# Kernel optimization log

Hardware: AMD Instinct MI355X
Metric: run time of the kernel (lower is better)

## Reference

```python
import jax, jax.numpy as jnp
import numpy as np

N, G = 10000, 200          # nodes, graphs
EL, EG = 160000, 500000    # local / global edges
S, V = 256, 64             # scalar / vector hidden dims
NA, NB = 16, 5             # atom types, bond types


def _lin(k, i, o):
    return (jax.random.normal(k, (i, o), jnp.float32) / np.sqrt(i))


def scatter_mean(vals, idx, num_segments):
    # vals: [N, ...]; idx: [N] int
    sums = jax.ops.segment_sum(vals, idx, num_segments=num_segments)
    cnt = jax.ops.segment_sum(jnp.ones((vals.shape[0],), vals.dtype), idx,
                              num_segments=num_segments)
    cnt = jnp.maximum(cnt, 1.0).reshape((-1,) + (1,) * (vals.ndim - 1))
    return sums / cnt


def calc_edge_attrs(edge_index, pos):
    src, tgt = edge_index[0], edge_index[1]
    r = pos[tgt] - pos[src]                      # [E,3]
    a = (pos[tgt] * pos[src]).sum(-1)            # [E]
    d = jnp.sqrt(jnp.clip((r ** 2).sum(-1), 1e-6))
    r_norm = r / d[:, None]
    return d, a, r_norm


def setup_inputs() -> dict:
    key = jax.random.key(0)
    ks = jax.random.split(key, 24)
    inp = {}
    inp["x"] = jax.random.normal(ks[0], (N, NA), jnp.float32)
    inp["t"] = jax.random.uniform(ks[1], (G, 1), jnp.float32)
    inp["pos"] = jax.random.normal(ks[2], (N, 3), jnp.float32)
    eil = jax.random.randint(ks[3], (2, EL), 0, N)
    eig = jax.random.randint(ks[4], (2, EG), 0, N)
    # avoid self-edges so edge distances are strictly positive (safe sqrt grads)
    eig = eig.at[1].set(jnp.where(eig[1] == eig[0], (eig[1] + 1) % N, eig[1]))
    eil = eil.at[1].set(jnp.where(eil[1] == eil[0], (eil[1] + 1) % N, eil[1]))
    inp["edge_index_local"] = eil
    inp["edge_index_global"] = eig
    inp["edge_attr_global"] = jax.random.normal(ks[5], (EG, NB), jnp.float32)
    inp["batch"] = jnp.sort(jax.random.randint(ks[6], (N,), 0, G))
    # learned parameters
    inp["W_time"], inp["b_time"] = _lin(ks[7], 1, S), jnp.zeros((S,), jnp.float32)
    inp["W_atom"], inp["b_atom"] = _lin(ks[8], NA, S), jnp.zeros((S,), jnp.float32)
    inp["W_at"], inp["b_at"] = _lin(ks[9], S, S), jnp.zeros((S,), jnp.float32)
    inp["W_shared"], inp["b_shared"] = _lin(ks[10], S, S), jnp.zeros((S,), jnp.float32)
    inp["W_b0"], inp["b_b0"] = _lin(ks[11], S + 1, S), jnp.zeros((S,), jnp.float32)
    inp["W_b1"], inp["b_b1"] = _lin(ks[12], S, 2 * NB), jnp.zeros((2 * NB,), jnp.float32)
    inp["W_coord"] = _lin(ks[13], V, 2)           # no bias
    inp["W_atoms"], inp["b_atoms"] = _lin(ks[14], S, 2 * NA), jnp.zeros((2 * NA,), jnp.float32)
    return inp


def reference(x, t, pos, edge_attr_global, W_time, b_time, W_atom, b_atom,
              W_at, b_at, W_shared, b_shared, W_b0, b_b0, W_b1, b_b1,
              W_coord, W_atoms, b_atoms,
              edge_index_local, edge_index_global, batch):
    # --- trunk: center positions, embed atoms + time ---
    pos = pos - scatter_mean(pos, batch, G)[batch]
    temb = t @ W_time + b_time                    # [G,S]
    tnode = temb[batch]                           # [N,S]
    s = x @ W_atom + b_atom
    s = (s + tnode) @ W_at + b_at                 # [N,S]
    # --- edge attrs (gather-compute pattern feeding the GNN) ---
    d_l, a_l, rn_l = calc_edge_attrs(edge_index_local, pos)
    d_g, a_g, rn_g = calc_edge_attrs(edge_index_global, pos)
    # GNN stand-in (identity on s, v, p): v initialized to zeros as in original
    v = jnp.zeros((N, 3, V), s.dtype)
    # --- prediction head ---
    s = jax.nn.silu(s @ W_shared + b_shared)
    j, i = edge_index_global[0], edge_index_global[1]
    d = jnp.sqrt(((pos[i] - pos[j]) ** 2).sum(-1, keepdims=True))  # [EG,1]
    edge = jnp.concatenate([s[i] + s[j], d], axis=-1)              # [EG,S+1]
    bonds = jax.nn.silu(edge @ W_b0 + b_b0) @ W_b1 + b_b1          # [EG,2*NB]
    bonds_pred, bonds_eps = bonds[:, :NB], bonds[:, NB:]
    coords = jnp.einsum('nkv,vo->nko', v, W_coord)                 # [N,3,2]
    coords = coords - scatter_mean(coords, batch, G)[batch]
    coords_eps0, coords_eps1 = coords[..., 0], coords[..., 1]      # [N,3]
    atoms = s @ W_atoms + b_atoms                                  # [N,2*NA]
    atoms_eps, atoms_pred = atoms[:, :NA], atoms[:, NA:]
    pos_c = pos - scatter_mean(pos, batch, G)[batch]
    coords_pred = pos_c + coords_eps1
    return (coords_pred, coords_eps0, atoms_pred, atoms_eps,
            bonds_pred, bonds_eps, d_l, rn_l, a_g, rn_g)
```

## Files before the change

kernel.cpp:

```cpp
#include <hip/hip_runtime.h>
#include <hip/hip_bf16.h>

typedef __hip_bfloat16 bf16;
typedef short bf16x8 __attribute__((ext_vector_type(8)));
typedef float f32x4 __attribute__((ext_vector_type(4)));
typedef float f32x2 __attribute__((ext_vector_type(2)));

#define N_NODES  10000
#define G_GRAPHS 200
#define EL_EDGES 160000
#define EG_EDGES 500000
#define S_DIM    256
#define APAD     264

#define BONDS_BLOCKS 15625
#define LOCAL_BLOCKS 625

#define WS_FLAG   0
#define WS_POSC   1024
#define WS_WD     31232
#define WS_BB0    31488
#define WS_BB1    34304
#define WS_WATOM  34560
#define WS_WTIME  38656
#define WS_BTIME  38912
#define WS_BATOM  39168
#define WS_BAT    39424
#define WS_BSH    39680
#define WS_BATOMS 39936
#define WS_T      40000
#define WS_X      40448
#define WT_AT     200448
#define WT_SH     233216
#define WT_B0     265984
#define WT_ATOMS  298752
#define WT_B1     302848
#define WS_H      304896
#define WS_END_FLOATS (WS_H + (N_NODES * S_DIM) / 4)

#define CHAN(S)    ((((S) >> 6) << 6) + (((S) & 3) << 4) + (((S) & 63) >> 2))
#define CHANINV(k) ((((k) >> 6) << 6) + (((k) & 15) << 2) + (((k) >> 4) & 3))

#define O_CPRED 0
#define O_CEPS  30000
#define O_APRED 60000
#define O_AEPS  220000
#define O_BPRED 380000
#define O_BEPS  2880000
#define O_DL    5380000
#define O_RNL   5540000
#define O_AG    6020000
#define O_RNG   6520000

__device__ __forceinline__ float b2f(bf16 v) { return __bfloat162float(v); }
__device__ __forceinline__ bf16  f2b(float v) { return __float2bfloat16(v); }
__device__ __forceinline__ unsigned short bbits(float v) {
    bf16 b = f2b(v);
    return *reinterpret_cast<unsigned short*>(&b);
}
__device__ __forceinline__ float ldin(const void* p, int idx, int isf32) {
    return isf32 ? ((const float*)p)[idx] : b2f(((const bf16*)p)[idx]);
}
__device__ __forceinline__ void stout(void* out, int f32o, size_t idx, float v) {
    if (f32o) ((float*)out)[idx] = v;
    else      ((bf16*)out)[idx]  = f2b(v);
}
__device__ __forceinline__ float silu(float p) {
    return p * __builtin_amdgcn_rcpf(1.0f + __expf(-p));
}
__device__ __forceinline__ int dtype_f32(const void* tt) {
    const unsigned short* q = (const unsigned short*)tt;
    int c = 0;
#pragma unroll
    for (int z = 0; z < 32; ++z) c += (q[z] >= 0x4000) ? 1 : 0;
    return c > 0;
}

__global__ void k_prep(const void* __restrict__ x, const void* __restrict__ tt,
                       const void* __restrict__ W_time, const void* __restrict__ b_time,
                       const void* __restrict__ W_atom, const void* __restrict__ b_atom,
                       const void* __restrict__ W_at, const void* __restrict__ b_at,
                       const void* __restrict__ W_shared, const void* __restrict__ b_shared,
                       const void* __restrict__ W_b0, const void* __restrict__ b_b0,
                       const void* __restrict__ W_b1, const void* __restrict__ b_b1,
                       const void* __restrict__ W_atoms, const void* __restrict__ b_atoms,
                       float* __restrict__ ws) {
    const int t = blockIdx.x * blockDim.x + threadIdx.x;
    const int f = dtype_f32(tt);
    if (t == 0) ws[WS_FLAG] = f ? 1.0f : 0.0f;
    if (t < 65536) {
        const int k = t >> 8, n = t & 255;
        ((unsigned short*)(ws + WT_AT))[n * 256 + k] = bbits(ldin(W_at, t, f));
        ((unsigned short*)(ws + WT_SH))[n * 256 + k] = bbits(ldin(W_shared, t, f));
        ((unsigned short*)(ws + WT_B0))[n * 256 + k] = bbits(ldin(W_b0, t, f));
    }
    if (t < 160000) ws[WS_X + t] = ldin(x, t, f);
    if (t < 8192) {
        const int k = t >> 5, n = t & 31;
        ((unsigned short*)(ws + WT_ATOMS))[n * 256 + k] = bbits(ldin(W_atoms, t, f));
    }
    if (t < 4096) ws[WS_WATOM + t] = ldin(W_atom, t, f);
    if (t < 2560) {
        const int k = t / 10, n = t - k * 10;
        ((unsigned short*)(ws + WT_B1))[n * 256 + CHANINV(k)] = bbits(ldin(W_b1, t, f));
    } else if (t < 4096) {
        ((unsigned short*)(ws + WT_B1))[t] = 0;
    }
    if (t < 256) {
        ws[WS_WD + t]    = ldin(W_b0, 65536 + CHAN(t), f);
        ws[WS_BB0 + t]   = ldin(b_b0, CHAN(t), f);
        ws[WS_WTIME + t] = ldin(W_time, t, f);
        ws[WS_BTIME + t] = ldin(b_time, t, f);
        ws[WS_BATOM + t] = ldin(b_atom, t, f);
        ws[WS_BAT + t]   = ldin(b_at, t, f);
        ws[WS_BSH + t]   = ldin(b_shared, t, f);
    }
    if (t < 200) ws[WS_T + t] = ldin(tt, t, f);
    if (t < 32)  ws[WS_BATOMS + t] = ldin(b_atoms, t, f);
    if (t < 16)  ws[WS_BB1 + t] = (t < 10) ? ldin(b_b1, t, f) : 0.0f;
}

__global__ void k_pos(const void* __restrict__ pos, const int* __restrict__ batch,
                      float* __restrict__ ws, void* __restrict__ out) {
    const int g = blockIdx.x;
    const int f32o = ws[WS_FLAG] != 0.0f;
    __shared__ int s_lo, s_hi;
    __shared__ float wsum[4][3];
    __shared__ float mean[3];
    if (threadIdx.x == 0) {
        int lo = 0, hi = N_NODES;
        while (lo < hi) { int m = (lo + hi) >> 1; if (batch[m] < g) lo = m + 1; else hi = m; }
        s_lo = lo;
        int lo2 = lo; hi = N_NODES;
        while (lo2 < hi) { int m = (lo2 + hi) >> 1; if (batch[m] < g + 1) lo2 = m + 1; else hi = m; }
        s_hi = lo2;
    }
    __syncthreads();
    const int lo = s_lo, hi = s_hi, cnt = hi - lo;
    float sx = 0.f, sy = 0.f, sz = 0.f;
    for (int n = lo + threadIdx.x; n < hi; n += 256) {
        sx += ldin(pos, n * 3 + 0, f32o);
        sy += ldin(pos, n * 3 + 1, f32o);
        sz += ldin(pos, n * 3 + 2, f32o);
    }
#pragma unroll
    for (int off = 32; off > 0; off >>= 1) {
        sx += __shfl_down(sx, off);
        sy += __shfl_down(sy, off);
        sz += __shfl_down(sz, off);
    }
    if ((threadIdx.x & 63) == 0) {
        wsum[threadIdx.x >> 6][0] = sx;
        wsum[threadIdx.x >> 6][1] = sy;
        wsum[threadIdx.x >> 6][2] = sz;
    }
    __syncthreads();
    if (threadIdx.x == 0) {
        float inv = 1.0f / (float)max(cnt, 1);
        mean[0] = (wsum[0][0] + wsum[1][0] + wsum[2][0] + wsum[3][0]) * inv;
        mean[1] = (wsum[0][1] + wsum[1][1] + wsum[2][1] + wsum[3][1]) * inv;
        mean[2] = (wsum[0][2] + wsum[1][2] + wsum[2][2] + wsum[3][2]) * inv;
    }
    __syncthreads();
    for (int n = lo + threadIdx.x; n < hi; n += 256) {
#pragma unroll
        for (int k = 0; k < 3; ++k) {
            float p = ldin(pos, n * 3 + k, f32o) - mean[k];
            ws[WS_POSC + n * 3 + k] = p;
            stout(out, f32o, O_CPRED + n * 3 + k, p);
            stout(out, f32o, O_CEPS + n * 3 + k, 0.0f);
        }
    }
}

__global__ __launch_bounds__(256) void k_node(
    const int* __restrict__ batch, const float* __restrict__ ws,
    unsigned int* __restrict__ h_out, void* __restrict__ out) {
    __shared__ unsigned short actA[16][APAD];
    __shared__ unsigned short actB[16][APAD];
    const int tid = threadIdx.x;
    const int wave = tid >> 6, lane = tid & 63;
    const int quad = lane >> 4, l16 = lane & 15;
    const int row0 = blockIdx.x * 16;

    {
        const int r = tid >> 4;
        const int c0 = (tid & 15) * 16;
        const int g = row0 + r;
        float tb = ws[WS_T + batch[g]];
        float xr[16];
#pragma unroll
        for (int k = 0; k < 16; ++k) xr[k] = ws[WS_X + g * 16 + k];
        for (int cc = 0; cc < 16; cc += 4) {
            const int c = c0 + cc;
            float a0 = ws[WS_BATOM + c + 0] + tb * ws[WS_WTIME + c + 0] + ws[WS_BTIME + c + 0];
            float a1 = ws[WS_BATOM + c + 1] + tb * ws[WS_WTIME + c + 1] + ws[WS_BTIME + c + 1];
            float a2 = ws[WS_BATOM + c + 2] + tb * ws[WS_WTIME + c + 2] + ws[WS_BTIME + c + 2];
            float a3 = ws[WS_BATOM + c + 3] + tb * ws[WS_WTIME + c + 3] + ws[WS_BTIME + c + 3];
#pragma unroll
            for (int k = 0; k < 16; ++k) {
                float4 w4 = *(const float4*)(ws + WS_WATOM + k * S_DIM + c);
                a0 += xr[k] * w4.x; a1 += xr[k] * w4.y;
                a2 += xr[k] * w4.z; a3 += xr[k] * w4.w;
            }
            actA[r][c + 0] = bbits(a0); actA[r][c + 1] = bbits(a1);
            actA[r][c + 2] = bbits(a2); actA[r][c + 3] = bbits(a3);
        }
    }
    __syncthreads();

    const unsigned short* wt_at = (const unsigned short*)(ws + WT_AT);
    const unsigned short* wt_sh = (const unsigned short*)(ws + WT_SH);
    const unsigned short* wt_b0 = (const unsigned short*)(ws + WT_B0);
    const unsigned short* wt_am = (const unsigned short*)(ws + WT_ATOMS);
    const int n0 = wave * 64;

    {
        f32x4 acc[4] = {};
        for (int kk = 0; kk < S_DIM; kk += 32) {
            const int k = kk + quad * 8;
            bf16x8 a = *(const bf16x8*)&actA[l16][k];
#pragma unroll
            for (int nt = 0; nt < 4; ++nt) {
                bf16x8 b = *(const bf16x8*)(wt_at + (size_t)(n0 + nt * 16 + l16) * S_DIM + k);
                acc[nt] = __builtin_amdgcn_mfma_f32_16x16x32_bf16(a, b, acc[nt], 0, 0, 0);
            }
        }
#pragma unroll
        for (int nt = 0; nt < 4; ++nt) {
            const int n = n0 + nt * 16 + l16;
            const float bv = ws[WS_BAT + n];
#pragma unroll
            for (int r = 0; r < 4; ++r)
                actB[quad * 4 + r][n] = bbits(acc[nt][r] + bv);
        }
    }
    __syncthreads();

    {
        f32x4 acc[4] = {};
        for (int kk = 0; kk < S_DIM; kk += 32) {
            const int k = kk + quad * 8;
            bf16x8 a = *(const bf16x8*)&actB[l16][k];
#pragma unroll
            for (int nt = 0; nt < 4; ++nt) {
                bf16x8 b = *(const bf16x8*)(wt_sh + (size_t)(n0 + nt * 16 + l16) * S_DIM + k);
                acc[nt] = __builtin_amdgcn_mfma_f32_16x16x32_bf16(a, b, acc[nt], 0, 0, 0);
            }
        }
        __syncthreads();
#pragma unroll
        for (int nt = 0; nt < 4; ++nt) {
            const int n = n0 + nt * 16 + l16;
            const float bv = ws[WS_BSH + n];
#pragma unroll
            for (int r = 0; r < 4; ++r)
                actA[quad * 4 + r][n] = bbits(silu(acc[nt][r] + bv));
        }
    }
    __syncthreads();

    {
        f32x4 acc[4] = {};
        for (int kk = 0; kk < S_DIM; kk += 32) {
            const int k = kk + quad * 8;
            bf16x8 a = *(const bf16x8*)&actA[l16][k];
#pragma unroll
            for (int nt = 0; nt < 4; ++nt) {
                bf16x8 b = *(const bf16x8*)(wt_b0 + (size_t)(n0 + nt * 16 + l16) * S_DIM + k);
                acc[nt] = __builtin_amdgcn_mfma_f32_16x16x32_bf16(a, b, acc[nt], 0, 0, 0);
            }
        }
#pragma unroll
        for (int r = 0; r < 4; ++r) {
            const int g = row0 + quad * 4 + r;
            int w = 0;
            w = __builtin_amdgcn_cvt_pk_fp8_f32(acc[0][r], acc[1][r], w, false);
            w = __builtin_amdgcn_cvt_pk_fp8_f32(acc[2][r], acc[3][r], w, true);
            h_out[(size_t)g * 64 + wave * 16 + l16] = (unsigned int)w;
        }
    }

    if (wave < 2) {
        f32x4 acc = {};
        const int n = wave * 16 + l16;
        for (int kk = 0; kk < S_DIM; kk += 32) {
            const int k = kk + quad * 8;
            bf16x8 a = *(const bf16x8*)&actA[l16][k];
            bf16x8 b = *(const bf16x8*)(wt_am + (size_t)n * S_DIM + k);
            acc = __builtin_amdgcn_mfma_f32_16x16x32_bf16(a, b, acc, 0, 0, 0);
        }
        const float bv = ws[WS_BATOMS + n];
        const int f32o = ws[WS_FLAG] != 0.0f;
#pragma unroll
        for (int r = 0; r < 4; ++r) {
            const int g = row0 + quad * 4 + r;
            float v = acc[r] + bv;
            if (n < 16) stout(out, f32o, O_AEPS + (size_t)g * 16 + n, v);
            else        stout(out, f32o, O_APRED + (size_t)g * 16 + (n - 16), v);
        }
    }
}

__global__ __launch_bounds__(256, 5) void k_edges(const int* __restrict__ eig,
                                                  const int* __restrict__ eil,
                                                  const float* __restrict__ ws,
                                                  const unsigned char* __restrict__ h,
                                                  void* __restrict__ out) {
    __shared__ unsigned char sm[2][32][272];
    __shared__ float cwd[256];
    __shared__ float cbb0[256];
    __shared__ unsigned short cwb1[16 * 264];
    const int f32o = ws[WS_FLAG] != 0.0f;

    if (blockIdx.x >= BONDS_BLOCKS) {
        const int e = (blockIdx.x - BONDS_BLOCKS) * 256 + threadIdx.x;
        const float* posc = ws + WS_POSC;
        const int s = eil[e];
        const int t = eil[EL_EDGES + e];
        float rx = posc[t * 3 + 0] - posc[s * 3 + 0];
        float ry = posc[t * 3 + 1] - posc[s * 3 + 1];
        float rz = posc[t * 3 + 2] - posc[s * 3 + 2];
        float dsq = rx * rx + ry * ry + rz * rz;
        float d = sqrtf(fmaxf(dsq, 1e-6f));
        float inv = 1.0f / d;
        stout(out, f32o, O_DL + e, d);
        stout(out, f32o, O_RNL + (size_t)e * 3 + 0, rx * inv);
        stout(out, f32o, O_RNL + (size_t)e * 3 + 1, ry * inv);
        stout(out, f32o, O_RNL + (size_t)e * 3 + 2, rz * inv);
        return;
    }

    {
        const int t = threadIdx.x;
        cwd[t]  = ws[WS_WD + t];
        cbb0[t] = ws[WS_BB0 + t];
        const unsigned short* wb1t = (const unsigned short*)(ws + WT_B1);
#pragma unroll
        for (int idx = 0; idx < 16; ++idx) {
            const int q = idx * 256 + t;
            cwb1[(q >> 8) * 264 + (q & 255)] = wb1t[q];
        }
    }

    const int wave = threadIdx.x >> 6, lane = threadIdx.x & 63;
    const int quad = lane >> 4, l16 = lane & 15;
    const int P = wave >> 1, sub = wave & 1;
    const int e0 = blockIdx.x * 32 + P * 16;

    uint4 tmp[4];
#pragma unroll
    for (int p = 0; p < 4; ++p) {
        const int r16 = p * 4 + quad;
        const int es = e0 + r16;
        const int node = sub ? eig[es] : eig[EG_EDGES + es];
        tmp[p] = *(const uint4*)(h + (size_t)node * 256 + l16 * 16);
    }
#pragma unroll
    for (int p = 0; p < 4; ++p) {
        const int row = sub * 16 + p * 4 + quad;
        *(uint4*)&sm[P][row][l16 * 16] = tmp[p];
    }

    if (sub == 0) {
        const int e = e0 + l16;
        const int j = eig[e];
        const int i = eig[EG_EDGES + e];
        const float* posc = ws + WS_POSC;
        float pix = posc[i * 3 + 0], piy = posc[i * 3 + 1], piz = posc[i * 3 + 2];
        float pjx = posc[j * 3 + 0], pjy = posc[j * 3 + 1], pjz = posc[j * 3 + 2];
        float rx = pix - pjx, ry = piy - pjy, rz = piz - pjz;
        float dsq = rx * rx + ry * ry + rz * rz;
        if (quad == 0) {
            float ag = pix * pjx + piy * pjy + piz * pjz;
            float inv = 1.0f / sqrtf(fmaxf(dsq, 1e-6f));
            stout(out, f32o, O_AG + e, ag);
            stout(out, f32o, O_RNG + (size_t)e * 3 + 0, rx * inv);
            stout(out, f32o, O_RNG + (size_t)e * 3 + 1, ry * inv);
            stout(out, f32o, O_RNG + (size_t)e * 3 + 2, rz * inv);
            *(float*)&sm[P][l16][256] = sqrtf(dsq);
        }
    }
    __syncthreads();

    const float d = *(const float*)&sm[P][l16][256];

    const int kbase = sub * 128;
    f32x4 acc = {};
#pragma unroll
    for (int t = 0; t < 4; ++t) {
        const int k = kbase + t * 32 + quad * 8;
        uint2 uaw = *(const uint2*)&sm[P][l16][k];
        uint2 ubw = *(const uint2*)&sm[P][16 + l16][k];
        float4 wA = *(const float4*)(cwd + k);
        float4 wB = *(const float4*)(cwd + k + 4);
        float4 bA = *(const float4*)(cbb0 + k);
        float4 bB = *(const float4*)(cbb0 + k + 4);
        f32x2 a01 = __builtin_amdgcn_cvt_pk_f32_fp8((int)uaw.x, false);
        f32x2 a23 = __builtin_amdgcn_cvt_pk_f32_fp8((int)uaw.x, true);
        f32x2 a45 = __builtin_amdgcn_cvt_pk_f32_fp8((int)uaw.y, false);
        f32x2 a67 = __builtin_amdgcn_cvt_pk_f32_fp8((int)uaw.y, true);
        f32x2 b01 = __builtin_amdgcn_cvt_pk_f32_fp8((int)ubw.x, false);
        f32x2 b23 = __builtin_amdgcn_cvt_pk_f32_fp8((int)ubw.x, true);
        f32x2 b45 = __builtin_amdgcn_cvt_pk_f32_fp8((int)ubw.y, false);
        f32x2 b67 = __builtin_amdgcn_cvt_pk_f32_fp8((int)ubw.y, true);
        union { bf16x8 v; unsigned short s[8]; } af;
        af.s[0] = bbits(silu(a01.x + b01.x + fmaf(d, wA.x, bA.x)));
        af.s[1] = bbits(silu(a01.y + b01.y + fmaf(d, wA.y, bA.y)));
        af.s[2] = bbits(silu(a23.x + b23.x + fmaf(d, wA.z, bA.z)));
        af.s[3] = bbits(silu(a23.y + b23.y + fmaf(d, wA.w, bA.w)));
        af.s[4] = bbits(silu(a45.x + b45.x + fmaf(d, wB.x, bB.x)));
        af.s[5] = bbits(silu(a45.y + b45.y + fmaf(d, wB.y, bB.y)));
        af.s[6] = bbits(silu(a67.x + b67.x + fmaf(d, wB.z, bB.z)));
        af.s[7] = bbits(silu(a67.y + b67.y + fmaf(d, wB.w, bB.w)));
        bf16x8 bfr = *(const bf16x8*)(cwb1 + (size_t)l16 * 264 + k);
        acc = __builtin_amdgcn_mfma_f32_16x16x32_bf16(af.v, bfr, acc, 0, 0, 0);
    }

    __syncthreads();
    f32x4* sc = (f32x4*)&sm[P][0][0];
    if (sub == 1) sc[lane] = acc;
    __syncthreads();
    if (sub == 0 && l16 < 10) {
        f32x4 o = sc[lane];
        const float bv = ws[WS_BB1 + l16];
#pragma unroll
        for (int r = 0; r < 4; ++r) {
            const int er = e0 + quad * 4 + r;
            float v = acc[r] + o[r] + bv;
            if (l16 < 5) stout(out, f32o, O_BPRED + (size_t)er * 5 + l16, v);
            else         stout(out, f32o, O_BEPS + (size_t)er * 5 + (l16 - 5), v);
        }
    }
}

extern "C" void kernel_launch(void* const* d_in, const int* in_sizes, int n_in,
                              void* d_out, int out_size, void* d_ws, size_t ws_size,
                              hipStream_t stream) {
    const void* x        = d_in[0];
    const void* t        = d_in[1];
    const void* pos      = d_in[2];
    const int*  eil      = (const int*)d_in[3];
    const int*  eig      = (const int*)d_in[4];
    const int*  batch    = (const int*)d_in[6];
    const void* W_time   = d_in[7];
    const void* b_time   = d_in[8];
    const void* W_atom   = d_in[9];
    const void* b_atom   = d_in[10];
    const void* W_at     = d_in[11];
    const void* b_at     = d_in[12];
    const void* W_shared = d_in[13];
    const void* b_shared = d_in[14];
    const void* W_b0     = d_in[15];
    const void* b_b0     = d_in[16];
    const void* W_b1     = d_in[17];
    const void* b_b1     = d_in[18];
    const void* W_atoms  = d_in[20];
    const void* b_atoms  = d_in[21];
    (void)in_sizes; (void)n_in; (void)out_size;

    const size_t NEED = (size_t)WS_END_FLOATS * sizeof(float);
    if (ws_size < NEED) return;

    float* ws = (float*)d_ws;
    unsigned int* hbuf = (unsigned int*)(ws + WS_H);

    k_prep<<<640, 256, 0, stream>>>(x, t, W_time, b_time, W_atom, b_atom,
                                    W_at, b_at, W_shared, b_shared, W_b0, b_b0,
                                    W_b1, b_b1, W_atoms, b_atoms, ws);
    k_pos<<<G_GRAPHS, 256, 0, stream>>>(pos, batch, ws, d_out);
    k_node<<<N_NODES / 16, 256, 0, stream>>>(batch, ws, hbuf, d_out);
    k_edges<<<BONDS_BLOCKS + LOCAL_BLOCKS, 256, 0, stream>>>(
        eig, eil, ws, (const unsigned char*)hbuf, d_out);
}
```

Measured before the change: 226.3 us.

## Switch bond second-layer MFMA to FP8 and fold b_b0 into node projections

```diff
diff --git a/kernel.cpp b/kernel.cpp
--- a/kernel.cpp
+++ b/kernel.cpp
@@ -15,11 +15,11 @@
 
 #define BONDS_BLOCKS 15625
 #define LOCAL_BLOCKS 625
+#define B1ROW    280
 
 #define WS_FLAG   0
 #define WS_POSC   1024
 #define WS_WD     31232
-#define WS_BB0    31488
 #define WS_BB1    34304
 #define WS_WATOM  34560
 #define WS_WTIME  38656
@@ -34,9 +34,10 @@
 #define WT_SH     233216
 #define WT_B0     265984
 #define WT_ATOMS  298752
-#define WT_B1     302848
-#define WS_H      304896
-#define WS_END_FLOATS (WS_H + (N_NODES * S_DIM) / 4)
+#define WS_B1F8   302848
+#define WS_H      303968
+#define WS_BB0R   943968
+#define WS_END_FLOATS 944224
 
 #define CHAN(S)    ((((S) >> 6) << 6) + (((S) & 3) << 4) + (((S) & 63) >> 2))
 #define CHANINV(k) ((((k) >> 6) << 6) + (((k) & 15) << 2) + (((k) >> 4) & 3))
@@ -99,16 +100,16 @@
         const int k = t >> 5, n = t & 31;
         ((unsigned short*)(ws + WT_ATOMS))[n * 256 + k] = bbits(ldin(W_atoms, t, f));
     }
+    if (t < 4480) {
+        const int n = t / B1ROW, s = t - n * B1ROW;
+        float v = (n < 10 && s < 256) ? ldin(W_b1, CHAN(s) * 10 + n, f) : 0.0f;
+        int enc = __builtin_amdgcn_cvt_pk_fp8_f32(v, 0.0f, 0, false);
+        ((unsigned char*)(ws + WS_B1F8))[t] = (unsigned char)(enc & 0xff);
+    }
     if (t < 4096) ws[WS_WATOM + t] = ldin(W_atom, t, f);
-    if (t < 2560) {
-        const int k = t / 10, n = t - k * 10;
-        ((unsigned short*)(ws + WT_B1))[n * 256 + CHANINV(k)] = bbits(ldin(W_b1, t, f));
-    } else if (t < 4096) {
-        ((unsigned short*)(ws + WT_B1))[t] = 0;
-    }
     if (t < 256) {
-        ws[WS_WD + t]    = ldin(W_b0, 65536 + CHAN(t), f);
-        ws[WS_BB0 + t]   = ldin(b_b0, CHAN(t), f);
+        ws[WS_WD + t]   = ldin(W_b0, 65536 + CHAN(t), f);
+        ws[WS_BB0R + t] = ldin(b_b0, t, f);
         ws[WS_WTIME + t] = ldin(W_time, t, f);
         ws[WS_BTIME + t] = ldin(b_time, t, f);
         ws[WS_BATOM + t] = ldin(b_atom, t, f);
@@ -271,12 +272,15 @@
                 acc[nt] = __builtin_amdgcn_mfma_f32_16x16x32_bf16(a, b, acc[nt], 0, 0, 0);
             }
         }
+        float bh[4];
+#pragma unroll
+        for (int nt = 0; nt < 4; ++nt) bh[nt] = 0.5f * ws[WS_BB0R + n0 + nt * 16 + l16];
 #pragma unroll
         for (int r = 0; r < 4; ++r) {
             const int g = row0 + quad * 4 + r;
             int w = 0;
-            w = __builtin_amdgcn_cvt_pk_fp8_f32(acc[0][r], acc[1][r], w, false);
-            w = __builtin_amdgcn_cvt_pk_fp8_f32(acc[2][r], acc[3][r], w, true);
+            w = __builtin_amdgcn_cvt_pk_fp8_f32(acc[0][r] + bh[0], acc[1][r] + bh[1], w, false);
+            w = __builtin_amdgcn_cvt_pk_fp8_f32(acc[2][r] + bh[2], acc[3][r] + bh[3], w, true);
             h_out[(size_t)g * 64 + wave * 16 + l16] = (unsigned int)w;
         }
     }
@@ -302,15 +306,15 @@
     }
 }
 
-__global__ __launch_bounds__(256, 5) void k_edges(const int* __restrict__ eig,
+__global__ __launch_bounds__(256, 7) void k_edges(const int* __restrict__ eig,
                                                   const int* __restrict__ eil,
                                                   const float* __restrict__ ws,
                                                   const unsigned char* __restrict__ h,
                                                   void* __restrict__ out) {
     __shared__ unsigned char sm[2][32][272];
     __shared__ float cwd[256];
-    __shared__ float cbb0[256];
-    __shared__ unsigned short cwb1[16 * 264];
+    __shared__ long cwb1l[16 * B1ROW / 8];
+    unsigned char* cwb1 = (unsigned char*)cwb1l;
     const int f32o = ws[WS_FLAG] != 0.0f;
 
     if (blockIdx.x >= BONDS_BLOCKS) {
@@ -333,14 +337,10 @@
 
     {
         const int t = threadIdx.x;
-        cwd[t]  = ws[WS_WD + t];
-        cbb0[t] = ws[WS_BB0 + t];
-        const unsigned short* wb1t = (const unsigned short*)(ws + WT_B1);
-#pragma unroll
-        for (int idx = 0; idx < 16; ++idx) {
-            const int q = idx * 256 + t;
-            cwb1[(q >> 8) * 264 + (q & 255)] = wb1t[q];
-        }
+        cwd[t] = ws[WS_WD + t];
+        const unsigned int* src = (const unsigned int*)(ws + WS_B1F8);
+        unsigned int* dst = (unsigned int*)cwb1;
+        for (int q = t; q < 16 * B1ROW / 4; q += 256) dst[q] = src[q];
     }
 
     const int wave = threadIdx.x >> 6, lane = threadIdx.x & 63;
@@ -384,6 +384,7 @@
     __syncthreads();
 
     const float d = *(const float*)&sm[P][l16][256];
+    const unsigned char* cw = cwb1 + (size_t)l16 * B1ROW;
 
     const int kbase = sub * 128;
     f32x4 acc = {};
@@ -394,8 +395,6 @@
         uint2 ubw = *(const uint2*)&sm[P][16 + l16][k];
         float4 wA = *(const float4*)(cwd + k);
         float4 wB = *(const float4*)(cwd + k + 4);
-        float4 bA = *(const float4*)(cbb0 + k);
-        float4 bB = *(const float4*)(cbb0 + k + 4);
         f32x2 a01 = __builtin_amdgcn_cvt_pk_f32_fp8((int)uaw.x, false);
         f32x2 a23 = __builtin_amdgcn_cvt_pk_f32_fp8((int)uaw.x, true);
         f32x2 a45 = __builtin_amdgcn_cvt_pk_f32_fp8((int)uaw.y, false);
@@ -404,17 +403,21 @@
         f32x2 b23 = __builtin_amdgcn_cvt_pk_f32_fp8((int)ubw.x, true);
         f32x2 b45 = __builtin_amdgcn_cvt_pk_f32_fp8((int)ubw.y, false);
         f32x2 b67 = __builtin_amdgcn_cvt_pk_f32_fp8((int)ubw.y, true);
-        union { bf16x8 v; unsigned short s[8]; } af;
-        af.s[0] = bbits(silu(a01.x + b01.x + fmaf(d, wA.x, bA.x)));
-        af.s[1] = bbits(silu(a01.y + b01.y + fmaf(d, wA.y, bA.y)));
-        af.s[2] = bbits(silu(a23.x + b23.x + fmaf(d, wA.z, bA.z)));
-        af.s[3] = bbits(silu(a23.y + b23.y + fmaf(d, wA.w, bA.w)));
-        af.s[4] = bbits(silu(a45.x + b45.x + fmaf(d, wB.x, bB.x)));
-        af.s[5] = bbits(silu(a45.y + b45.y + fmaf(d, wB.y, bB.y)));
-        af.s[6] = bbits(silu(a67.x + b67.x + fmaf(d, wB.z, bB.z)));
-        af.s[7] = bbits(silu(a67.y + b67.y + fmaf(d, wB.w, bB.w)));
-        bf16x8 bfr = *(const bf16x8*)(cwb1 + (size_t)l16 * 264 + k);
-        acc = __builtin_amdgcn_mfma_f32_16x16x32_bf16(af.v, bfr, acc, 0, 0, 0);
+        float u0 = silu(fmaf(d, wA.x, a01.x + b01.x));
+        float u1 = silu(fmaf(d, wA.y, a01.y + b01.y));
+        float u2 = silu(fmaf(d, wA.z, a23.x + b23.x));
+        float u3 = silu(fmaf(d, wA.w, a23.y + b23.y));
+        float u4 = silu(fmaf(d, wB.x, a45.x + b45.x));
+        float u5 = silu(fmaf(d, wB.y, a45.y + b45.y));
+        float u6 = silu(fmaf(d, wB.z, a67.x + b67.x));
+        float u7 = silu(fmaf(d, wB.w, a67.y + b67.y));
+        int lo = __builtin_amdgcn_cvt_pk_fp8_f32(u0, u1, 0, false);
+        lo = __builtin_amdgcn_cvt_pk_fp8_f32(u2, u3, lo, true);
+        int hi = __builtin_amdgcn_cvt_pk_fp8_f32(u4, u5, 0, false);
+        hi = __builtin_amdgcn_cvt_pk_fp8_f32(u6, u7, hi, true);
+        long a64 = (long)(((unsigned long)(unsigned int)hi << 32) | (unsigned int)lo);
+        long b64 = *(const long*)(cw + k);
+        acc = __builtin_amdgcn_mfma_f32_16x16x32_fp8_fp8(a64, b64, acc, 0, 0, 0);
     }
 
     __syncthreads();
```

Result: no change. 222.7 us (-1.6%).
